# Kernel tuning notes

Hardware: AMD Instinct MI355X
Metric: run time of the kernel (lower is better)

## Reference

```python
import jax, jax.numpy as jnp
import numpy as np
import math

Z, N = 4, 128
EMB, L0, MLPH, GEO = 16, 32, 64, 64
NB, NH = 32, 128
C = MLPH + GEO
BETA, MAXR = 5.0, 10.0
Y0 = 0.5 / math.sqrt(math.pi)  # spherical harmonic l=0


def setup_inputs() -> dict:
    key = jax.random.key(0)
    ks = jax.random.split(key, 24)
    g = lambda i, s: jax.random.normal(ks[i], s, jnp.float32)
    inp = {}
    inp['features'] = jax.random.randint(ks[0], (Z, N, 1), 0, 6)
    inp['geometry'] = g(1, (Z, N, 3))
    inp['mask'] = jnp.ones((Z, N), jnp.float32)
    emb = g(2, (6, EMB))
    inp['emb'] = emb.at[5].set(0.0)  # padding_idx=5
    # radial MLP weights per conv layer (basis->h->h->mul_out*mul_in)
    inp['r0w0'] = g(3, (NB, NH)); inp['r0w1'] = g(4, (NH, NH)); inp['r0w2'] = g(5, (NH, L0 * EMB))
    inp['r1w0'] = g(6, (NB, NH)); inp['r1w1'] = g(7, (NH, NH)); inp['r1w2'] = g(8, (NH, L0 * L0))
    inp['r2w0'] = g(9, (NB, NH)); inp['r2w1'] = g(10, (NH, NH)); inp['r2w2'] = g(11, (NH, MLPH * L0))
    # ResnetPointnet (3 -> GEO per atom, two residual FC blocks)
    inp['pn_w0'] = g(12, (3, GEO)) * 0.3; inp['pn_b0'] = jnp.zeros((GEO,), jnp.float32)
    inp['pn_w1a'] = g(13, (GEO, GEO)) * 0.1; inp['pn_b1a'] = jnp.zeros((GEO,), jnp.float32)
    inp['pn_w1b'] = g(14, (GEO, GEO)) * 0.1; inp['pn_b1b'] = jnp.zeros((GEO,), jnp.float32)
    inp['pn_w2a'] = g(15, (GEO, GEO)) * 0.1; inp['pn_b2a'] = jnp.zeros((GEO,), jnp.float32)
    inp['pn_w2b'] = g(16, (GEO, GEO)) * 0.1; inp['pn_b2b'] = jnp.zeros((GEO,), jnp.float32)
    # output MLP + per-atom BatchNorm1d(natoms) params
    inp['e1_w'] = g(17, (C, C)) * 0.05; inp['e1_b'] = jnp.zeros((C,), jnp.float32)
    inp['bn1_g'] = jnp.ones((N,), jnp.float32); inp['bn1_b'] = jnp.zeros((N,), jnp.float32)
    inp['e2_w'] = g(18, (C, 2 * C)) * 0.05; inp['e2_b'] = jnp.zeros((2 * C,), jnp.float32)
    inp['bn2_g'] = jnp.ones((N,), jnp.float32); inp['bn2_b'] = jnp.zeros((N,), jnp.float32)
    return inp


def _sp(x):
    return jax.nn.softplus(BETA * x) / BETA


def _ssp(x):
    return _sp(x) - math.log(2.0) / BETA


def _leaky(x):
    return jnp.where(x > 0, x, 0.2 * x)


def _radial(radii, w0, w1, w2):
    # CosineBasisModel: smooth cosine^2 bumps then small MLP (e3nn-style /sqrt(fan_in))
    centers = jnp.linspace(0.0, MAXR, NB)
    step = centers[1] - centers[0]
    x = (radii[..., None] - centers) / step
    basis = jnp.where(jnp.abs(x) < 1.0, jnp.cos(0.5 * jnp.pi * x) ** 2, 0.0)  # [z,a,b,NB]
    h = _ssp(basis @ w0 / math.sqrt(NB))
    h = _ssp(h @ w1 / math.sqrt(NH))
    return h @ w2 / math.sqrt(NH)  # [z,a,b,dout*din]


def _bn(x, gamma, beta):
    # torch BatchNorm1d(natoms) on [Z, natoms, C]: normalize over (Z, C) per atom slot
    mu = jnp.mean(x, axis=(0, 2), keepdims=True)
    var = jnp.var(x, axis=(0, 2), keepdims=True)
    xn = (x - mu) * jax.lax.rsqrt(var + 1e-5)
    return xn * gamma[None, :, None] + beta[None, :, None]


def reference(features, geometry, mask, emb,
              r0w0, r0w1, r0w2, r1w0, r1w1, r1w2, r2w0, r2w1, r2w2,
              pn_w0, pn_b0, pn_w1a, pn_b1a, pn_w1b, pn_b1b,
              pn_w2a, pn_b2a, pn_w2b, pn_b2b,
              e1_w, e1_b, bn1_g, bn1_b, e2_w, e2_b, bn2_g, bn2_b):
    # constants(): pairwise geometry, detached in the original
    diff = jax.lax.stop_gradient(geometry[:, None, :, :] - geometry[:, :, None, :])  # [z,a,b,3]
    radii = jnp.linalg.norm(diff, axis=-1)  # [z,a,b]

    # ResnetPointnet: per-atom geometric features
    net = geometry @ pn_w0 + pn_b0
    for (wa, ba, wb, bb) in ((pn_w1a, pn_b1a, pn_w1b, pn_b1b), (pn_w2a, pn_b2a, pn_w2b, pn_b2b)):
        dx = jax.nn.relu(net) @ wa + ba
        dx = jax.nn.relu(dx) @ wb + bb
        net = net + dx
    geo_pn = net * mask[..., None]  # [z,n,GEO]

    # embedding
    f = emb[features[..., 0]]  # [z,n,EMB]

    # equivariant kernel-conv layers; all reps are l=0 so Y = Y0 constant
    dims = ((EMB, L0, r0w0, r0w1, r0w2), (L0, L0, r1w0, r1w1, r1w2), (L0, MLPH, r2w0, r2w1, r2w2))
    for (din, dout, w0, w1, w2) in dims:
        f = f / math.sqrt(N)
        K = _radial(radii, w0, w1, w2).reshape(Z, N, N, dout, din)
        f = jnp.einsum('zabij,zbj,zb->zai', K, f, mask) * Y0
        f = _sp(f)               # GatedBlock with all-scalar Rs -> scalar act only
        f = f * mask[..., None]

    feat = jnp.concatenate([f, geo_pn], axis=2)  # [z,n,C]
    x = _leaky(_bn(feat @ e1_w + e1_b, bn1_g, bn1_b))
    x = _leaky(_bn(x @ e2_w + e2_b, bn2_g, bn2_b))
    out = jnp.sum(x * mask[..., None], axis=1)  # Aggregate(axis=1, sum)
    return out  # [Z, 2*C]
```

## Files before the change

kernel.cpp:

```cpp
#include <hip/hip_runtime.h>
#include <math.h>

#define Zc   4
#define Nc   128
#define EMBc 16
#define L0c  32
#define MLPHc 64
#define GEOc 64
#define NBc  32
#define NHc  128
#define Cc   128
#define SLc  64

typedef float  f32x4  __attribute__((ext_vector_type(4)));
typedef short  bf16x8 __attribute__((ext_vector_type(8)));

union FragU {
    bf16x8 v;
    unsigned short u[8];
    uint2 q2[2];
};

__device__ __forceinline__ float sp5(float x){
    float y = 5.0f * x;
    float t = fabsf(y);
    return (fmaxf(y, 0.0f) + log1pf(__expf(-t))) * 0.2f;
}
__device__ __forceinline__ float ssp5_post(float y){
    float e = __expf(-fabsf(y));
    float u = fmaxf(y, 0.0f) + __logf(1.0f + e);
    return fmaf(0.2f, u, -0.13862943611198906f);
}

__device__ __forceinline__ unsigned int cvtpk_bf16(float a, float b){
    unsigned int r;
    asm("v_cvt_pk_bf16_f32 %0, %1, %2" : "=v"(r) : "v"(a), "v"(b));
    return r;
}
__device__ __forceinline__ unsigned short f2bf(float f){
    unsigned int u = __float_as_uint(f);
    unsigned int r = (u + 0x7FFFu + ((u >> 16) & 1u)) >> 16;
    return (unsigned short)r;
}

__device__ __forceinline__ int kmap(int l, int e){
    return 4*((l >> 4) & 3) + (e & 3) + 16*(e >> 2);
}

__global__ __launch_bounds__(256) void k_init(
    const float* __restrict__ geom, const float* __restrict__ mask,
    const float* __restrict__ pw0, const float* __restrict__ pb0,
    const float* __restrict__ w1a, const float* __restrict__ b1a,
    const float* __restrict__ w1b, const float* __restrict__ b1b,
    const float* __restrict__ w2a, const float* __restrict__ b2a,
    const float* __restrict__ w2b, const float* __restrict__ b2b,
    const int*   __restrict__ features, const float* __restrict__ emb,
    const float* __restrict__ w00, const float* __restrict__ w10,
    const float* __restrict__ w01, const float* __restrict__ w11,
    const float* __restrict__ w02, const float* __restrict__ w12,
    float* __restrict__ geo_pn, float* __restrict__ f0,
    unsigned short* __restrict__ packs, float* __restrict__ outz)
{
    __shared__ float cur[4][GEOc];
    __shared__ float tmp[4][GEOc];
    int bx = blockIdx.x;
    int t  = threadIdx.x;
    if (bx < 128){
        int g  = t >> 6;
        int c  = t & 63;
        int zn = bx*4 + g;
        float gx = geom[zn*3+0], gy = geom[zn*3+1], gz = geom[zn*3+2];
        float v = fmaf(gx, pw0[0*GEOc+c], fmaf(gy, pw0[1*GEOc+c], fmaf(gz, pw0[2*GEOc+c], pb0[c])));
        const float* WA[2] = {w1a, w2a}; const float* BA[2] = {b1a, b2a};
        const float* WB[2] = {w1b, w2b}; const float* BB[2] = {b1b, b2b};
        #pragma unroll
        for (int blk = 0; blk < 2; blk++){
            cur[g][c] = v;
            __syncthreads();
            float s = BA[blk][c];
            for (int k = 0; k < GEOc; k++) s = fmaf(fmaxf(cur[g][k], 0.0f), WA[blk][k*GEOc+c], s);
            tmp[g][c] = s;
            __syncthreads();
            float s2 = BB[blk][c];
            for (int k = 0; k < GEOc; k++) s2 = fmaf(fmaxf(tmp[g][k], 0.0f), WB[blk][k*GEOc+c], s2);
            v = v + s2;
            __syncthreads();
        }
        geo_pn[zn*GEOc + c] = v * mask[zn];
        if (c < EMBc){
            int fi = features[zn];
            f0[zn*EMBc + c] = emb[fi*EMBc + c] * mask[zn] * 0.0022038655607334227f;
        }
    } else if (bx < 368){
        int j = bx - 128;
        int layer = j / 80;
        int sub = j % 80;
        const float* w0s = (layer == 0) ? w00 : (layer == 1) ? w01 : w02;
        const float* w1s = (layer == 0) ? w10 : (layer == 1) ? w11 : w12;
        unsigned short* p0 = packs + layer*4096;
        unsigned short* p1 = packs + 12288 + layer*16384;
        int idx = sub*256 + t;
        if (idx < 4096){
            int t8 = idx >> 9, l = (idx >> 3) & 63, e = idx & 7;
            int k = kmap(l, e);
            int n = (t8 << 4) + (l & 15);
            p0[idx] = f2bf(w0s[k*NHc + n] * 0.8838834764831844f);
        } else {
            int jj = idx - 4096;
            int fid = jj >> 9, l = (jj >> 3) & 63, e = jj & 7;
            int kk = fid >> 3, t8 = fid & 7;
            int k = 32*kk + kmap(l, e);
            int n = 16*t8 + (l & 15);
            p1[jj] = f2bf(w1s[k*NHc + n] * 0.4419417382415922f);
        }
    } else {
        for (int i = t; i < Zc*2*Cc; i += 256) outz[i] = 0.0f;
    }
}

template<int DIN, int DOUT>
__global__ __launch_bounds__(256) void k_gmat(
    const float* __restrict__ f, const float* __restrict__ w2,
    unsigned short* __restrict__ gt)
{
    __shared__ float fsh[8][DIN];
    int t   = threadIdx.x;
    int zb0 = blockIdx.x * 8;
    if (t < 8*DIN){
        int r = t / DIN, j = t % DIN;
        fsh[r][j] = f[(zb0 + r)*DIN + j];
    }
    __syncthreads();
    int mi = blockIdx.y * 256 + t;
    int m_ = mi & (NHc-1);
    int i_ = mi >> 7;
    const float* wrow = w2 + (size_t)(m_*DOUT + i_) * DIN;
    float s[8];
    #pragma unroll
    for (int r = 0; r < 8; r++) s[r] = 0.0f;
    #pragma unroll
    for (int j4 = 0; j4 < DIN/4; j4++){
        float4 w = *reinterpret_cast<const float4*>(&wrow[j4*4]);
        #pragma unroll
        for (int q = 0; q < 4; q++){
            float wv = reinterpret_cast<const float*>(&w)[q];
            int j = j4*4 + q;
            #pragma unroll
            for (int r = 0; r < 8; r++)
                s[r] = fmaf(fsh[r][j], wv, s[r]);
        }
    }
    int z = zb0 >> 7;
    #pragma unroll
    for (int r = 0; r < 8; r++){
        int b = (zb0 + r) & (Nc-1);
        gt[((size_t)z*DOUT + i_)*(Nc*NHc) + b*NHc + m_] = (unsigned short)cvtpk_bf16(s[r], s[r]);
    }
}

template<int DIN, int DOUT>
__global__ __launch_bounds__(256) void k_egmat(
    const float* __restrict__ part, const float* __restrict__ mask,
    const float* __restrict__ w2, unsigned short* __restrict__ gt)
{
    __shared__ float fsh[8][DIN];
    int t   = threadIdx.x;
    int zb0 = blockIdx.x * 8;
    for (int idx = t; idx < 8*DIN; idx += 256){
        int r = idx / DIN, j = idx % DIN;
        int zb = zb0 + r;
        float s = 0.0f;
        #pragma unroll
        for (int sl = 0; sl < SLc; sl++)
            s += part[(size_t)sl*(Zc*Nc*DIN) + zb*DIN + j];
        float m = mask[zb];
        fsh[r][j] = sp5(s) * m * m * 0.0022038655607334227f;
    }
    __syncthreads();
    int mi = blockIdx.y * 256 + t;
    int m_ = mi & (NHc-1);
    int i_ = mi >> 7;
    const float* wrow = w2 + (size_t)(m_*DOUT + i_) * DIN;
    float s[8];
    #pragma unroll
    for (int r = 0; r < 8; r++) s[r] = 0.0f;
    #pragma unroll
    for (int j4 = 0; j4 < DIN/4; j4++){
        float4 w = *reinterpret_cast<const float4*>(&wrow[j4*4]);
        #pragma unroll
        for (int q = 0; q < 4; q++){
            float wv = reinterpret_cast<const float*>(&w)[q];
            int j = j4*4 + q;
            #pragma unroll
            for (int r = 0; r < 8; r++)
                s[r] = fmaf(fsh[r][j], wv, s[r]);
        }
    }
    int z = zb0 >> 7;
    #pragma unroll
    for (int r = 0; r < 8; r++){
        int b = (zb0 + r) & (Nc-1);
        gt[((size_t)z*DOUT + i_)*(Nc*NHc) + b*NHc + m_] = (unsigned short)cvtpk_bf16(s[r], s[r]);
    }
}

__global__ __launch_bounds__(256, 2) void k_pairmlp(
    const float* __restrict__ geom,
    const unsigned short* __restrict__ packs,
    unsigned short* __restrict__ h2all)
{
    __shared__ unsigned short h1s[64*128];
    char* lb = (char*)h1s;
    int t   = threadIdx.x;
    int w   = t >> 6;
    int l   = t & 63;
    int g16 = l >> 4;
    int c   = l & 15;
    int p0  = blockIdx.x * 64;
    int z   = p0 >> 14;
    int a   = (p0 >> 7) & 127;
    int b0  = p0 & 127;

    if (b0 + 16*w + 15 < a) return;

    int layer = blockIdx.y;
    const unsigned short* wp0 = packs + layer*4096;
    const unsigned short* wp1 = packs + 12288 + layer*16384;
    unsigned short* h2 = h2all + (size_t)layer * (Zc*Nc*Nc*NHc);

    int bp = b0 + 16*w + c;
    float ax = geom[(z*Nc + a)*3 + 0];
    float ay = geom[(z*Nc + a)*3 + 1];
    float az = geom[(z*Nc + a)*3 + 2];
    float dx = geom[(z*Nc + bp)*3 + 0] - ax;
    float dy = geom[(z*Nc + bp)*3 + 1] - ay;
    float dz = geom[(z*Nc + bp)*3 + 2] - az;
    float rm = sqrtf(dx*dx + dy*dy + dz*dz);

    FragU af;
    #pragma unroll
    for (int e = 0; e < 8; e++){
        int k = kmap(l, e);
        float x = fmaf(rm, 3.1f, -(float)k);
        float v = 0.0f;
        if (fabsf(x) < 1.0f){ float cc = __cosf(1.57079632679f*x); v = cc*cc; }
        af.u[e] = (unsigned short)cvtpk_bf16(v, v);
    }

    f32x4 acc[8];
    #pragma unroll
    for (int t8 = 0; t8 < 8; t8++) acc[t8] = (f32x4){0.f,0.f,0.f,0.f};
    #pragma unroll
    for (int t8 = 0; t8 < 8; t8++){
        bf16x8 bf = *reinterpret_cast<const bf16x8*>(wp0 + ((t8*64 + l) << 3));
        acc[t8] = __builtin_amdgcn_mfma_f32_16x16x32_bf16(af.v, bf, acc[t8], 0, 0, 0);
    }
    #pragma unroll
    for (int t8 = 0; t8 < 8; t8++){
        #pragma unroll
        for (int rg = 0; rg < 4; rg++){
            int m = 16*w + 4*g16 + rg;
            int n = 16*t8 + c;
            int off = ((m << 8) + (n << 1)) ^ ((m & 7) << 4);
            *(unsigned short*)(lb + off) = (unsigned short)cvtpk_bf16(ssp5_post(acc[t8][rg]), 0.0f);
        }
    }

    f32x4 acc2[8];
    #pragma unroll
    for (int t8 = 0; t8 < 8; t8++) acc2[t8] = (f32x4){0.f,0.f,0.f,0.f};
    int mrow = 16*w + c;
    int sw   = (mrow & 7) << 4;
    #pragma unroll
    for (int kk = 0; kk < 4; kk++){
        int ob = (mrow << 8) + (kk << 6) + (g16 << 3);
        FragU a2;
        a2.q2[0] = *(const uint2*)(lb + (ob ^ sw));
        a2.q2[1] = *(const uint2*)(lb + ((ob + 32) ^ sw));
        #pragma unroll
        for (int t8 = 0; t8 < 8; t8++){
            bf16x8 bf = *reinterpret_cast<const bf16x8*>(wp1 + (((kk*8 + t8)*64 + l) << 3));
            acc2[t8] = __builtin_amdgcn_mfma_f32_16x16x32_bf16(a2.v, bf, acc2[t8], 0, 0, 0);
        }
    }
    size_t zbase = (size_t)z*Nc*Nc*NHc;
    #pragma unroll
    for (int t8 = 0; t8 < 8; t8++){
        #pragma unroll
        for (int rg = 0; rg < 4; rg++){
            int m = 16*w + 4*g16 + rg;
            int b = b0 + m;
            unsigned short val = (unsigned short)cvtpk_bf16(ssp5_post(acc2[t8][rg]), 0.0f);
            h2[zbase + ((size_t)a*Nc + b)*NHc + 16*t8 + c] = val;
            if (b > a)
                h2[zbase + ((size_t)b*Nc + a)*NHc + 16*t8 + c] = val;
        }
    }
}

template<int DOUT>
__global__ __launch_bounds__(256) void k_gemm3m(
    const unsigned short* __restrict__ h2, const unsigned short* __restrict__ gt,
    float* __restrict__ partial)
{
    __shared__ unsigned short Ash[64*256];
    __shared__ unsigned short Bsh[DOUT*256];
    int t = threadIdx.x;
    int w = t >> 6, l = t & 63;
    int g16 = l >> 4, c16 = l & 15;
    int s  = blockIdx.x;
    int at = blockIdx.y;
    int z  = blockIdx.z;
    int a0 = at*64;
    int k0 = s*256;

    {
        const unsigned short* src = h2 + ((size_t)(z*Nc + a0))*(Nc*NHc) + k0;
        #pragma unroll
        for (int it = 0; it < 8; it++){
            int idx = it*256 + t;
            int r = idx >> 5, c8 = idx & 31;
            uint4 v = *reinterpret_cast<const uint4*>(src + (size_t)r*(Nc*NHc) + c8*8);
            int byte = (r*512 + c8*16) ^ ((r & 7) << 4);
            *reinterpret_cast<uint4*>((char*)Ash + byte) = v;
        }
    }
    {
        const unsigned short* src = gt + ((size_t)z*DOUT)*(Nc*NHc) + k0;
        #pragma unroll
        for (int it = 0; it < DOUT/8; it++){
            int idx = it*256 + t;
            int r = idx >> 5, c8 = idx & 31;
            uint4 v = *reinterpret_cast<const uint4*>(src + (size_t)r*(Nc*NHc) + c8*8);
            int byte = (r*512 + c8*16) ^ ((r & 7) << 4);
            *reinterpret_cast<uint4*>((char*)Bsh + byte) = v;
        }
    }
    __syncthreads();

    constexpr int NT = DOUT/16;
    f32x4 acc[NT];
    #pragma unroll
    for (int nt = 0; nt < NT; nt++) acc[nt] = (f32x4){0.f,0.f,0.f,0.f};
    char* Ab = (char*)Ash; char* Bb = (char*)Bsh;
    int ar  = 16*w + c16;
    int asw = (ar & 7) << 4;
    #pragma unroll
    for (int ks = 0; ks < 8; ks++){
        FragU afr;
        int abyte = ar*512 + ks*64 + g16*8;
        afr.q2[0] = *(const uint2*)(Ab + (abyte ^ asw));
        afr.q2[1] = *(const uint2*)(Ab + ((abyte + 32) ^ asw));
        #pragma unroll
        for (int nt = 0; nt < NT; nt++){
            int br  = nt*16 + c16;
            int bsw = (br & 7) << 4;
            int bbyte = br*512 + ks*64 + g16*8;
            FragU bfr;
            bfr.q2[0] = *(const uint2*)(Bb + (bbyte ^ bsw));
            bfr.q2[1] = *(const uint2*)(Bb + ((bbyte + 32) ^ bsw));
            acc[nt] = __builtin_amdgcn_mfma_f32_16x16x32_bf16(afr.v, bfr.v, acc[nt], 0, 0, 0);
        }
    }
    #pragma unroll
    for (int nt = 0; nt < NT; nt++){
        #pragma unroll
        for (int rg = 0; rg < 4; rg++){
            int a = a0 + 16*w + 4*g16 + rg;
            int i = nt*16 + c16;
            partial[(((size_t)s*Zc + z)*Nc + a)*DOUT + i] = acc[nt][rg];
        }
    }
}

__global__ __launch_bounds__(256) void k_tail(
    const float* __restrict__ part, const float* __restrict__ mask,
    const float* __restrict__ geo_pn,
    const float* __restrict__ e1w, const float* __restrict__ e1b,
    const float* __restrict__ g1, const float* __restrict__ b1,
    const float* __restrict__ e2w, const float* __restrict__ e2b,
    const float* __restrict__ g2, const float* __restrict__ b2,
    float* __restrict__ outp)
{
    int n = blockIdx.x;
    int t = threadIdx.x;
    __shared__ float feat[Zc][Cc];
    __shared__ float xln[Zc][Cc];
    __shared__ float r1[4], r2[4];

    {
        int z = t >> 6, i = t & 63;
        float s = 0.0f;
        #pragma unroll
        for (int sl = 0; sl < SLc; sl++)
            s += part[((size_t)sl*Zc*Nc + z*Nc + n)*MLPHc + i];
        float m = mask[z*Nc + n];
        feat[z][i] = sp5(s) * m;
        feat[z][MLPHc + i] = geo_pn[(z*Nc + n)*GEOc + i];
    }
    __syncthreads();

    int c  = t & 127;
    int zh = t >> 7;
    float x1v[2];
    float sum = 0.0f, sq = 0.0f;
    #pragma unroll
    for (int q = 0; q < 2; q++){
        int z = zh*2 + q;
        float s = e1b[c];
        for (int k = 0; k < Cc; k++) s = fmaf(feat[z][k], e1w[k*Cc + c], s);
        x1v[q] = s; sum += s; sq = fmaf(s, s, sq);
    }
    #pragma unroll
    for (int off = 32; off > 0; off >>= 1){
        sum += __shfl_down(sum, off);
        sq  += __shfl_down(sq,  off);
    }
    if ((t & 63) == 0){ r1[t >> 6] = sum; r2[t >> 6] = sq; }
    __syncthreads();
    {
        float tot  = r1[0]+r1[1]+r1[2]+r1[3];
        float totq = r2[0]+r2[1]+r2[2]+r2[3];
        float mu   = tot * (1.0f/512.0f);
        float var  = totq * (1.0f/512.0f) - mu*mu;
        float rstd = rsqrtf(var + 1e-5f);
        float ga = g1[n], be = b1[n];
        #pragma unroll
        for (int q = 0; q < 2; q++){
            float v = (x1v[q] - mu) * rstd * ga + be;
            xln[zh*2 + q][c] = v > 0.0f ? v : 0.2f*v;
        }
    }
    __syncthreads();

    float x2v[4];
    sum = 0.0f; sq = 0.0f;
    #pragma unroll
    for (int z = 0; z < Zc; z++){
        float s = e2b[t];
        for (int k = 0; k < Cc; k++) s = fmaf(xln[z][k], e2w[k*2*Cc + t], s);
        x2v[z] = s; sum += s; sq = fmaf(s, s, sq);
    }
    #pragma unroll
    for (int off = 32; off > 0; off >>= 1){
        sum += __shfl_down(sum, off);
        sq  += __shfl_down(sq,  off);
    }
    if ((t & 63) == 0){ r1[t >> 6] = sum; r2[t >> 6] = sq; }
    __syncthreads();
    {
        float tot  = r1[0]+r1[1]+r1[2]+r1[3];
        float totq = r2[0]+r2[1]+r2[2]+r2[3];
        float mu   = tot * (1.0f/1024.0f);
        float var  = totq * (1.0f/1024.0f) - mu*mu;
        float rstd = rsqrtf(var + 1e-5f);
        float ga = g2[n], be = b2[n];
        #pragma unroll
        for (int z = 0; z < Zc; z++){
            float v = (x2v[z] - mu) * rstd * ga + be;
            v = v > 0.0f ? v : 0.2f*v;
            atomicAdd(&outp[z*2*Cc + t], v * mask[z*Nc + n]);
        }
    }
}

extern "C" void kernel_launch(void* const* d_in, const int* in_sizes, int n_in,
                              void* d_out, int out_size, void* d_ws, size_t ws_size,
                              hipStream_t stream)
{
    const int*   features = (const int*)  d_in[0];
    const float* geom     = (const float*)d_in[1];
    const float* mask     = (const float*)d_in[2];
    const float* emb      = (const float*)d_in[3];
    const float* rw[3][3] = {
        {(const float*)d_in[4],  (const float*)d_in[5],  (const float*)d_in[6]},
        {(const float*)d_in[7],  (const float*)d_in[8],  (const float*)d_in[9]},
        {(const float*)d_in[10], (const float*)d_in[11], (const float*)d_in[12]}};
    const float* pw0 = (const float*)d_in[13]; const float* pb0 = (const float*)d_in[14];
    const float* w1a = (const float*)d_in[15]; const float* b1a = (const float*)d_in[16];
    const float* w1b = (const float*)d_in[17]; const float* b1b = (const float*)d_in[18];
    const float* w2a = (const float*)d_in[19]; const float* b2a = (const float*)d_in[20];
    const float* w2b = (const float*)d_in[21]; const float* b2b = (const float*)d_in[22];
    const float* e1w = (const float*)d_in[23]; const float* e1b = (const float*)d_in[24];
    const float* bn1g= (const float*)d_in[25]; const float* bn1b= (const float*)d_in[26];
    const float* e2w = (const float*)d_in[27]; const float* e2b = (const float*)d_in[28];
    const float* bn2g= (const float*)d_in[29]; const float* bn2b= (const float*)d_in[30];

    float* ws = (float*)d_ws;
    unsigned short* h2buf = (unsigned short*)ws;
    unsigned short* gt    = (unsigned short*)(ws + 12582912);
    float* part   = ws + 12582912 + 2097152;
    float* f0     = part + 2097152;
    float* geo_pn = f0 + 8192;
    unsigned short* packs = (unsigned short*)(geo_pn + 32768);
    (void)ws_size; (void)in_sizes; (void)n_in; (void)out_size;

    const size_t H2L = (size_t)Zc*Nc*Nc*NHc;

    k_init<<<369, 256, 0, stream>>>(geom, mask, pw0, pb0, w1a, b1a, w1b, b1b,
                                    w2a, b2a, w2b, b2b, features, emb,
                                    rw[0][0], rw[0][1], rw[1][0], rw[1][1],
                                    rw[2][0], rw[2][1],
                                    geo_pn, f0, packs, (float*)d_out);
    k_pairmlp<<<dim3(Zc*Nc*Nc/64, 3), 256, 0, stream>>>(geom, packs, h2buf);

    k_gmat<16,32><<<dim3(Zc*Nc/8, (NHc*32)/256), 256, 0, stream>>>(f0, rw[0][2], gt);
    k_gemm3m<32><<<dim3(SLc,2,Zc), 256, 0, stream>>>(h2buf, gt, part);
    k_egmat<32,32><<<dim3(Zc*Nc/8, (NHc*32)/256), 256, 0, stream>>>(part, mask, rw[1][2], gt);
    k_gemm3m<32><<<dim3(SLc,2,Zc), 256, 0, stream>>>(h2buf + H2L, gt, part);
    k_egmat<32,64><<<dim3(Zc*Nc/8, (NHc*64)/256), 256, 0, stream>>>(part, mask, rw[2][2], gt);
    k_gemm3m<64><<<dim3(SLc,2,Zc), 256, 0, stream>>>(h2buf + 2*H2L, gt, part);

    k_tail<<<Nc, 256, 0, stream>>>(part, mask, geo_pn, e1w, e1b, bn1g, bn1b,
                                   e2w, e2b, bn2g, bn2b, (float*)d_out);
}
```

Before: 152.3 us.

## Fuse all stages into one cooperative persistent kernel with grid syncs

Replaces the nine separate kernel launches with a single cooperative kernel of 512 blocks. The blocks loop over virtual block indices for each stage and separate the stages with grid.sync(), which removes the per-launch gaps and tail effects between small stages. The K-split of the h2·G GEMM is also halved from 256 to 128 columns, which gives 128 partial slices. That means more, smaller GEMM blocks, a doubled partial buffer and twice as many partials to reduce in the egmat and tail stages. If cooperative launch is unavailable, the code falls back to the multi-kernel path.

```diff
diff --git a/kernel.cpp b/kernel.cpp
--- a/kernel.cpp
+++ b/kernel.cpp
@@ -1,5 +1,8 @@
 #include <hip/hip_runtime.h>
+#include <hip/hip_cooperative_groups.h>
 #include <math.h>
+
+namespace cg = cooperative_groups;
 
 #define Zc   4
 #define Nc   128
@@ -10,7 +13,8 @@
 #define NBc  32
 #define NHc  128
 #define Cc   128
-#define SLc  64
+#define SLc  128
+#define SL2  128
 
 typedef float  f32x4  __attribute__((ext_vector_type(4)));
 typedef short  bf16x8 __attribute__((ext_vector_type(8)));
@@ -21,6 +25,16 @@
     uint2 q2[2];
 };
 
+struct P {
+    const float *geom, *mask, *emb;
+    const int*   features;
+    const float *pw0,*pb0,*w1a,*b1a,*w1b,*b1b,*w2a,*b2a,*w2b,*b2b;
+    const float *r00,*r01,*r02, *r10,*r11,*r12, *r20,*r21,*r22;
+    const float *e1w,*e1b,*bn1g,*bn1b,*e2w,*e2b,*bn2g,*bn2b;
+    unsigned short *h2buf, *gt, *packs;
+    float *part, *f0, *geo_pn, *outp;
+};
+
 __device__ __forceinline__ float sp5(float x){
     float y = 5.0f * x;
     float t = fabsf(y);
@@ -31,7 +45,6 @@
     float u = fmaxf(y, 0.0f) + __logf(1.0f + e);
     return fmaf(0.2f, u, -0.13862943611198906f);
 }
-
 __device__ __forceinline__ unsigned int cvtpk_bf16(float a, float b){
     unsigned int r;
     asm("v_cvt_pk_bf16_f32 %0, %1, %2" : "=v"(r) : "v"(a), "v"(b));
@@ -42,63 +55,52 @@
     unsigned int r = (u + 0x7FFFu + ((u >> 16) & 1u)) >> 16;
     return (unsigned short)r;
 }
-
 __device__ __forceinline__ int kmap(int l, int e){
     return 4*((l >> 4) & 3) + (e & 3) + 16*(e >> 2);
 }
 
-__global__ __launch_bounds__(256) void k_init(
-    const float* __restrict__ geom, const float* __restrict__ mask,
-    const float* __restrict__ pw0, const float* __restrict__ pb0,
-    const float* __restrict__ w1a, const float* __restrict__ b1a,
-    const float* __restrict__ w1b, const float* __restrict__ b1b,
-    const float* __restrict__ w2a, const float* __restrict__ b2a,
-    const float* __restrict__ w2b, const float* __restrict__ b2b,
-    const int*   __restrict__ features, const float* __restrict__ emb,
-    const float* __restrict__ w00, const float* __restrict__ w10,
-    const float* __restrict__ w01, const float* __restrict__ w11,
-    const float* __restrict__ w02, const float* __restrict__ w12,
-    float* __restrict__ geo_pn, float* __restrict__ f0,
-    unsigned short* __restrict__ packs, float* __restrict__ outz)
-{
-    __shared__ float cur[4][GEOc];
-    __shared__ float tmp[4][GEOc];
-    int bx = blockIdx.x;
-    int t  = threadIdx.x;
+__device__ void init_dev(int bx, const P& p, char* smem)
+{
+    float* cur = (float*)smem;
+    float* tmp = cur + 4*GEOc;
+    int t = threadIdx.x;
     if (bx < 128){
         int g  = t >> 6;
         int c  = t & 63;
         int zn = bx*4 + g;
-        float gx = geom[zn*3+0], gy = geom[zn*3+1], gz = geom[zn*3+2];
-        float v = fmaf(gx, pw0[0*GEOc+c], fmaf(gy, pw0[1*GEOc+c], fmaf(gz, pw0[2*GEOc+c], pb0[c])));
-        const float* WA[2] = {w1a, w2a}; const float* BA[2] = {b1a, b2a};
-        const float* WB[2] = {w1b, w2b}; const float* BB[2] = {b1b, b2b};
+        float gx = p.geom[zn*3+0], gy = p.geom[zn*3+1], gz = p.geom[zn*3+2];
+        float v = fmaf(gx, p.pw0[0*GEOc+c], fmaf(gy, p.pw0[1*GEOc+c],
+                  fmaf(gz, p.pw0[2*GEOc+c], p.pb0[c])));
+        const float* WA[2] = {p.w1a, p.w2a}; const float* BA[2] = {p.b1a, p.b2a};
+        const float* WB[2] = {p.w1b, p.w2b}; const float* BB[2] = {p.b1b, p.b2b};
         #pragma unroll
         for (int blk = 0; blk < 2; blk++){
-            cur[g][c] = v;
+            cur[g*GEOc + c] = v;
             __syncthreads();
             float s = BA[blk][c];
-            for (int k = 0; k < GEOc; k++) s = fmaf(fmaxf(cur[g][k], 0.0f), WA[blk][k*GEOc+c], s);
-            tmp[g][c] = s;
+            for (int k = 0; k < GEOc; k++)
+                s = fmaf(fmaxf(cur[g*GEOc + k], 0.0f), WA[blk][k*GEOc+c], s);
+            tmp[g*GEOc + c] = s;
             __syncthreads();
             float s2 = BB[blk][c];
-            for (int k = 0; k < GEOc; k++) s2 = fmaf(fmaxf(tmp[g][k], 0.0f), WB[blk][k*GEOc+c], s2);
+            for (int k = 0; k < GEOc; k++)
+                s2 = fmaf(fmaxf(tmp[g*GEOc + k], 0.0f), WB[blk][k*GEOc+c], s2);
             v = v + s2;
             __syncthreads();
         }
-        geo_pn[zn*GEOc + c] = v * mask[zn];
+        p.geo_pn[zn*GEOc + c] = v * p.mask[zn];
         if (c < EMBc){
-            int fi = features[zn];
-            f0[zn*EMBc + c] = emb[fi*EMBc + c] * mask[zn] * 0.0022038655607334227f;
+            int fi = p.features[zn];
+            p.f0[zn*EMBc + c] = p.emb[fi*EMBc + c] * p.mask[zn] * 0.0022038655607334227f;
         }
     } else if (bx < 368){
         int j = bx - 128;
         int layer = j / 80;
         int sub = j % 80;
-        const float* w0s = (layer == 0) ? w00 : (layer == 1) ? w01 : w02;
-        const float* w1s = (layer == 0) ? w10 : (layer == 1) ? w11 : w12;
-        unsigned short* p0 = packs + layer*4096;
-        unsigned short* p1 = packs + 12288 + layer*16384;
+        const float* w0s = (layer == 0) ? p.r00 : (layer == 1) ? p.r10 : p.r20;
+        const float* w1s = (layer == 0) ? p.r01 : (layer == 1) ? p.r11 : p.r21;
+        unsigned short* p0 = p.packs + layer*4096;
+        unsigned short* p1 = p.packs + 12288 + layer*16384;
         int idx = sub*256 + t;
         if (idx < 4096){
             int t8 = idx >> 9, l = (idx >> 3) & 63, e = idx & 7;
@@ -114,127 +116,37 @@
             p1[jj] = f2bf(w1s[k*NHc + n] * 0.4419417382415922f);
         }
     } else {
-        for (int i = t; i < Zc*2*Cc; i += 256) outz[i] = 0.0f;
-    }
-}
-
-template<int DIN, int DOUT>
-__global__ __launch_bounds__(256) void k_gmat(
-    const float* __restrict__ f, const float* __restrict__ w2,
-    unsigned short* __restrict__ gt)
-{
-    __shared__ float fsh[8][DIN];
-    int t   = threadIdx.x;
-    int zb0 = blockIdx.x * 8;
-    if (t < 8*DIN){
-        int r = t / DIN, j = t % DIN;
-        fsh[r][j] = f[(zb0 + r)*DIN + j];
-    }
-    __syncthreads();
-    int mi = blockIdx.y * 256 + t;
-    int m_ = mi & (NHc-1);
-    int i_ = mi >> 7;
-    const float* wrow = w2 + (size_t)(m_*DOUT + i_) * DIN;
-    float s[8];
-    #pragma unroll
-    for (int r = 0; r < 8; r++) s[r] = 0.0f;
-    #pragma unroll
-    for (int j4 = 0; j4 < DIN/4; j4++){
-        float4 w = *reinterpret_cast<const float4*>(&wrow[j4*4]);
-        #pragma unroll
-        for (int q = 0; q < 4; q++){
-            float wv = reinterpret_cast<const float*>(&w)[q];
-            int j = j4*4 + q;
-            #pragma unroll
-            for (int r = 0; r < 8; r++)
-                s[r] = fmaf(fsh[r][j], wv, s[r]);
-        }
-    }
-    int z = zb0 >> 7;
-    #pragma unroll
-    for (int r = 0; r < 8; r++){
-        int b = (zb0 + r) & (Nc-1);
-        gt[((size_t)z*DOUT + i_)*(Nc*NHc) + b*NHc + m_] = (unsigned short)cvtpk_bf16(s[r], s[r]);
-    }
-}
-
-template<int DIN, int DOUT>
-__global__ __launch_bounds__(256) void k_egmat(
-    const float* __restrict__ part, const float* __restrict__ mask,
-    const float* __restrict__ w2, unsigned short* __restrict__ gt)
-{
-    __shared__ float fsh[8][DIN];
-    int t   = threadIdx.x;
-    int zb0 = blockIdx.x * 8;
-    for (int idx = t; idx < 8*DIN; idx += 256){
-        int r = idx / DIN, j = idx % DIN;
-        int zb = zb0 + r;
-        float s = 0.0f;
-        #pragma unroll
-        for (int sl = 0; sl < SLc; sl++)
-            s += part[(size_t)sl*(Zc*Nc*DIN) + zb*DIN + j];
-        float m = mask[zb];
-        fsh[r][j] = sp5(s) * m * m * 0.0022038655607334227f;
-    }
-    __syncthreads();
-    int mi = blockIdx.y * 256 + t;
-    int m_ = mi & (NHc-1);
-    int i_ = mi >> 7;
-    const float* wrow = w2 + (size_t)(m_*DOUT + i_) * DIN;
-    float s[8];
-    #pragma unroll
-    for (int r = 0; r < 8; r++) s[r] = 0.0f;
-    #pragma unroll
-    for (int j4 = 0; j4 < DIN/4; j4++){
-        float4 w = *reinterpret_cast<const float4*>(&wrow[j4*4]);
-        #pragma unroll
-        for (int q = 0; q < 4; q++){
-            float wv = reinterpret_cast<const float*>(&w)[q];
-            int j = j4*4 + q;
-            #pragma unroll
-            for (int r = 0; r < 8; r++)
-                s[r] = fmaf(fsh[r][j], wv, s[r]);
-        }
-    }
-    int z = zb0 >> 7;
-    #pragma unroll
-    for (int r = 0; r < 8; r++){
-        int b = (zb0 + r) & (Nc-1);
-        gt[((size_t)z*DOUT + i_)*(Nc*NHc) + b*NHc + m_] = (unsigned short)cvtpk_bf16(s[r], s[r]);
-    }
-}
-
-__global__ __launch_bounds__(256, 2) void k_pairmlp(
-    const float* __restrict__ geom,
-    const unsigned short* __restrict__ packs,
-    unsigned short* __restrict__ h2all)
-{
-    __shared__ unsigned short h1s[64*128];
-    char* lb = (char*)h1s;
+        for (int i = t; i < Zc*2*Cc; i += 256) p.outp[i] = 0.0f;
+    }
+}
+
+__device__ void pairmlp_dev(int vb, const P& p, char* smem)
+{
+    char* lb = smem;
     int t   = threadIdx.x;
     int w   = t >> 6;
     int l   = t & 63;
     int g16 = l >> 4;
     int c   = l & 15;
-    int p0  = blockIdx.x * 64;
+    int layer = vb >> 10;
+    int p0  = (vb & 1023) * 64;
     int z   = p0 >> 14;
     int a   = (p0 >> 7) & 127;
     int b0  = p0 & 127;
 
     if (b0 + 16*w + 15 < a) return;
 
-    int layer = blockIdx.y;
-    const unsigned short* wp0 = packs + layer*4096;
-    const unsigned short* wp1 = packs + 12288 + layer*16384;
-    unsigned short* h2 = h2all + (size_t)layer * (Zc*Nc*Nc*NHc);
+    const unsigned short* wp0 = p.packs + layer*4096;
+    const unsigned short* wp1 = p.packs + 12288 + layer*16384;
+    unsigned short* h2 = p.h2buf + (size_t)layer * ((size_t)Zc*Nc*Nc*NHc);
 
     int bp = b0 + 16*w + c;
-    float ax = geom[(z*Nc + a)*3 + 0];
-    float ay = geom[(z*Nc + a)*3 + 1];
-    float az = geom[(z*Nc + a)*3 + 2];
-    float dx = geom[(z*Nc + bp)*3 + 0] - ax;
-    float dy = geom[(z*Nc + bp)*3 + 1] - ay;
-    float dz = geom[(z*Nc + bp)*3 + 2] - az;
+    float ax = p.geom[(z*Nc + a)*3 + 0];
+    float ay = p.geom[(z*Nc + a)*3 + 1];
+    float az = p.geom[(z*Nc + a)*3 + 2];
+    float dx = p.geom[(z*Nc + bp)*3 + 0] - ax;
+    float dy = p.geom[(z*Nc + bp)*3 + 1] - ay;
+    float dz = p.geom[(z*Nc + bp)*3 + 2] - az;
     float rm = sqrtf(dx*dx + dy*dy + dz*dz);
 
     FragU af;
@@ -298,41 +210,131 @@
     }
 }
 
-template<int DOUT>
-__global__ __launch_bounds__(256) void k_gemm3m(
-    const unsigned short* __restrict__ h2, const unsigned short* __restrict__ gt,
-    float* __restrict__ partial)
-{
-    __shared__ unsigned short Ash[64*256];
-    __shared__ unsigned short Bsh[DOUT*256];
+template<int DIN, int DOUT>
+__device__ void gmat_dev(int vb, const float* f, const float* w2,
+                         unsigned short* gt, char* smem)
+{
+    float (*fsh)[DIN] = (float (*)[DIN])smem;
+    int t  = threadIdx.x;
+    int bx = vb & 63, by = vb >> 6;
+    int zb0 = bx * 8;
+    if (t < 8*DIN){
+        int r = t / DIN, j = t % DIN;
+        fsh[r][j] = f[(zb0 + r)*DIN + j];
+    }
+    __syncthreads();
+    int mi = by * 256 + t;
+    int m_ = mi & (NHc-1);
+    int i_ = mi >> 7;
+    const float* wrow = w2 + (size_t)(m_*DOUT + i_) * DIN;
+    float s[8];
+    #pragma unroll
+    for (int r = 0; r < 8; r++) s[r] = 0.0f;
+    #pragma unroll
+    for (int j4 = 0; j4 < DIN/4; j4++){
+        float4 wv4 = *reinterpret_cast<const float4*>(&wrow[j4*4]);
+        #pragma unroll
+        for (int q = 0; q < 4; q++){
+            float wv = reinterpret_cast<const float*>(&wv4)[q];
+            int j = j4*4 + q;
+            #pragma unroll
+            for (int r = 0; r < 8; r++)
+                s[r] = fmaf(fsh[r][j], wv, s[r]);
+        }
+    }
+    int z = zb0 >> 7;
+    #pragma unroll
+    for (int r = 0; r < 8; r++){
+        int b = (zb0 + r) & (Nc-1);
+        gt[((size_t)z*DOUT + i_)*(Nc*NHc) + b*NHc + m_] = (unsigned short)cvtpk_bf16(s[r], s[r]);
+    }
+    __syncthreads();
+}
+
+template<int DIN, int DOUT>
+__device__ void egmat_dev(int vb, const float* part, const float* mask,
+                          const float* w2, unsigned short* gt, char* smem)
+{
+    float (*fsh)[DIN] = (float (*)[DIN])smem;
+    int t  = threadIdx.x;
+    int bx = vb & 63, by = vb >> 6;
+    int zb0 = bx * 8;
+    for (int idx = t; idx < 8*DIN; idx += 256){
+        int r = idx / DIN, j = idx % DIN;
+        int zb = zb0 + r;
+        float s = 0.0f;
+        for (int sl = 0; sl < SLc; sl++)
+            s += part[(size_t)sl*(Zc*Nc*DIN) + zb*DIN + j];
+        float m = mask[zb];
+        fsh[r][j] = sp5(s) * m * m * 0.0022038655607334227f;
+    }
+    __syncthreads();
+    int mi = by * 256 + t;
+    int m_ = mi & (NHc-1);
+    int i_ = mi >> 7;
+    const float* wrow = w2 + (size_t)(m_*DOUT + i_) * DIN;
+    float s[8];
+    #pragma unroll
+    for (int r = 0; r < 8; r++) s[r] = 0.0f;
+    #pragma unroll
+    for (int j4 = 0; j4 < DIN/4; j4++){
+        float4 wv4 = *reinterpret_cast<const float4*>(&wrow[j4*4]);
+        #pragma unroll
+        for (int q = 0; q < 4; q++){
+            float wv = reinterpret_cast<const float*>(&wv4)[q];
+            int j = j4*4 + q;
+            #pragma unroll
+            for (int r = 0; r < 8; r++)
+                s[r] = fmaf(fsh[r][j], wv, s[r]);
+        }
+    }
+    int z = zb0 >> 7;
+    #pragma unroll
+    for (int r = 0; r < 8; r++){
+        int b = (zb0 + r) & (Nc-1);
+        gt[((size_t)z*DOUT + i_)*(Nc*NHc) + b*NHc + m_] = (unsigned short)cvtpk_bf16(s[r], s[r]);
+    }
+    __syncthreads();
+}
+
+template<int DOUT, int KS>
+__device__ void gemm3_dev(int vb, const unsigned short* h2, const unsigned short* gt,
+                          float* partial, char* smem)
+{
+    constexpr int NS   = (Nc*NHc)/KS;
+    constexpr int ROWB = KS*2;
+    unsigned short* Ash = (unsigned short*)smem;
+    unsigned short* Bsh = (unsigned short*)(smem + 64*ROWB);
     int t = threadIdx.x;
     int w = t >> 6, l = t & 63;
     int g16 = l >> 4, c16 = l & 15;
-    int s  = blockIdx.x;
-    int at = blockIdx.y;
-    int z  = blockIdx.z;
+    int s  = vb % NS;
+    int at = (vb / NS) & 1;
+    int z  = vb / (NS*2);
     int a0 = at*64;
-    int k0 = s*256;
+    int k0 = s*KS;
 
     {
         const unsigned short* src = h2 + ((size_t)(z*Nc + a0))*(Nc*NHc) + k0;
-        #pragma unroll
-        for (int it = 0; it < 8; it++){
+        constexpr int ITA = (64*(KS/8))/256;
+        #pragma unroll
+        for (int it = 0; it < ITA; it++){
             int idx = it*256 + t;
-            int r = idx >> 5, c8 = idx & 31;
+            int r = idx / (KS/8), c8 = idx % (KS/8);
             uint4 v = *reinterpret_cast<const uint4*>(src + (size_t)r*(Nc*NHc) + c8*8);
-            int byte = (r*512 + c8*16) ^ ((r & 7) << 4);
+            int byte = (r*ROWB + c8*16) ^ ((r & 7) << 4);
             *reinterpret_cast<uint4*>((char*)Ash + byte) = v;
         }
     }
     {
         const unsigned short* src = gt + ((size_t)z*DOUT)*(Nc*NHc) + k0;
-        #pragma unroll
-        for (int it = 0; it < DOUT/8; it++){
+        constexpr int ITB = (DOUT*(KS/8))/256;
+        #pragma unroll
+        for (int it = 0; it < ITB; it++){
             int idx = it*256 + t;
-            int r = idx >> 5, c8 = idx & 31;
+            int r = idx / (KS/8), c8 = idx % (KS/8);
             uint4 v = *reinterpret_cast<const uint4*>(src + (size_t)r*(Nc*NHc) + c8*8);
-            int byte = (r*512 + c8*16) ^ ((r & 7) << 4);
+            int byte = (r*ROWB + c8*16) ^ ((r & 7) << 4);
             *reinterpret_cast<uint4*>((char*)Bsh + byte) = v;
         }
     }
@@ -342,23 +344,22 @@
     f32x4 acc[NT];
     #pragma unroll
     for (int nt = 0; nt < NT; nt++) acc[nt] = (f32x4){0.f,0.f,0.f,0.f};
-    char* Ab = (char*)Ash; char* Bb = (char*)Bsh;
     int ar  = 16*w + c16;
     int asw = (ar & 7) << 4;
     #pragma unroll
-    for (int ks = 0; ks < 8; ks++){
+    for (int ks = 0; ks < KS/32; ks++){
         FragU afr;
-        int abyte = ar*512 + ks*64 + g16*8;
-        afr.q2[0] = *(const uint2*)(Ab + (abyte ^ asw));
-        afr.q2[1] = *(const uint2*)(Ab + ((abyte + 32) ^ asw));
+        int abyte = ar*ROWB + ks*64 + g16*8;
+        afr.q2[0] = *(const uint2*)((char*)Ash + (abyte ^ asw));
+        afr.q2[1] = *(const uint2*)((char*)Ash + ((abyte + 32) ^ asw));
         #pragma unroll
         for (int nt = 0; nt < NT; nt++){
             int br  = nt*16 + c16;
             int bsw = (br & 7) << 4;
-            int bbyte = br*512 + ks*64 + g16*8;
+            int bbyte = br*ROWB + ks*64 + g16*8;
             FragU bfr;
-            bfr.q2[0] = *(const uint2*)(Bb + (bbyte ^ bsw));
-            bfr.q2[1] = *(const uint2*)(Bb + ((bbyte + 32) ^ bsw));
+            bfr.q2[0] = *(const uint2*)((char*)Bsh + (bbyte ^ bsw));
+            bfr.q2[1] = *(const uint2*)((char*)Bsh + ((bbyte + 32) ^ bsw));
             acc[nt] = __builtin_amdgcn_mfma_f32_16x16x32_bf16(afr.v, bfr.v, acc[nt], 0, 0, 0);
         }
     }
@@ -371,32 +372,25 @@
             partial[(((size_t)s*Zc + z)*Nc + a)*DOUT + i] = acc[nt][rg];
         }
     }
-}
-
-__global__ __launch_bounds__(256) void k_tail(
-    const float* __restrict__ part, const float* __restrict__ mask,
-    const float* __restrict__ geo_pn,
-    const float* __restrict__ e1w, const float* __restrict__ e1b,
-    const float* __restrict__ g1, const float* __restrict__ b1,
-    const float* __restrict__ e2w, const float* __restrict__ e2b,
-    const float* __restrict__ g2, const float* __restrict__ b2,
-    float* __restrict__ outp)
-{
-    int n = blockIdx.x;
+    __syncthreads();
+}
+
+__device__ void tail_dev(int n, const P& p, char* smem)
+{
+    float* feat = (float*)smem;
+    float* xln  = feat + Zc*Cc;
+    float* r1   = xln + Zc*Cc;
+    float* r2   = r1 + 4;
     int t = threadIdx.x;
-    __shared__ float feat[Zc][Cc];
-    __shared__ float xln[Zc][Cc];
-    __shared__ float r1[4], r2[4];
 
     {
         int z = t >> 6, i = t & 63;
         float s = 0.0f;
-        #pragma unroll
-        for (int sl = 0; sl < SLc; sl++)
-            s += part[((size_t)sl*Zc*Nc + z*Nc + n)*MLPHc + i];
-        float m = mask[z*Nc + n];
-        feat[z][i] = sp5(s) * m;
-        feat[z][MLPHc + i] = geo_pn[(z*Nc + n)*GEOc + i];
+        for (int sl = 0; sl < SL2; sl++)
+            s += p.part[((size_t)sl*Zc*Nc + z*Nc + n)*MLPHc + i];
+        float m = p.mask[z*Nc + n];
+        feat[z*Cc + i] = sp5(s) * m;
+        feat[z*Cc + MLPHc + i] = p.geo_pn[(z*Nc + n)*GEOc + i];
     }
     __syncthreads();
 
@@ -407,8 +401,8 @@
     #pragma unroll
     for (int q = 0; q < 2; q++){
         int z = zh*2 + q;
-        float s = e1b[c];
-        for (int k = 0; k < Cc; k++) s = fmaf(feat[z][k], e1w[k*Cc + c], s);
+        float s = p.e1b[c];
+        for (int k = 0; k < Cc; k++) s = fmaf(feat[z*Cc + k], p.e1w[k*Cc + c], s);
         x1v[q] = s; sum += s; sq = fmaf(s, s, sq);
     }
     #pragma unroll
@@ -424,11 +418,11 @@
         float mu   = tot * (1.0f/512.0f);
         float var  = totq * (1.0f/512.0f) - mu*mu;
         float rstd = rsqrtf(var + 1e-5f);
-        float ga = g1[n], be = b1[n];
+        float ga = p.bn1g[n], be = p.bn1b[n];
         #pragma unroll
         for (int q = 0; q < 2; q++){
             float v = (x1v[q] - mu) * rstd * ga + be;
-            xln[zh*2 + q][c] = v > 0.0f ? v : 0.2f*v;
+            xln[(zh*2 + q)*Cc + c] = v > 0.0f ? v : 0.2f*v;
         }
     }
     __syncthreads();
@@ -437,8 +431,8 @@
     sum = 0.0f; sq = 0.0f;
     #pragma unroll
     for (int z = 0; z < Zc; z++){
-        float s = e2b[t];
-        for (int k = 0; k < Cc; k++) s = fmaf(xln[z][k], e2w[k*2*Cc + t], s);
+        float s = p.e2b[t];
+        for (int k = 0; k < Cc; k++) s = fmaf(xln[z*Cc + k], p.e2w[k*2*Cc + t], s);
         x2v[z] = s; sum += s; sq = fmaf(s, s, sq);
     }
     #pragma unroll
@@ -454,63 +448,129 @@
         float mu   = tot * (1.0f/1024.0f);
         float var  = totq * (1.0f/1024.0f) - mu*mu;
         float rstd = rsqrtf(var + 1e-5f);
-        float ga = g2[n], be = b2[n];
+        float ga = p.bn2g[n], be = p.bn2b[n];
         #pragma unroll
         for (int z = 0; z < Zc; z++){
             float v = (x2v[z] - mu) * rstd * ga + be;
             v = v > 0.0f ? v : 0.2f*v;
-            atomicAdd(&outp[z*2*Cc + t], v * mask[z*Nc + n]);
-        }
-    }
+            atomicAdd(&p.outp[z*2*Cc + t], v * p.mask[z*Nc + n]);
+        }
+    }
+}
+
+__global__ __launch_bounds__(256, 2) void k_mono(P p)
+{
+    __shared__ __align__(16) char smem[32768];
+    cg::grid_group grid = cg::this_grid();
+    const size_t H2L = (size_t)Zc*Nc*Nc*NHc;
+    int bid = blockIdx.x;
+
+    if (bid < 369) init_dev(bid, p, smem);
+    grid.sync();
+
+    for (int vb = bid; vb < 3072; vb += 512) pairmlp_dev(vb, p, smem);
+    grid.sync();
+
+    for (int vb = bid; vb < 1024; vb += 512) gmat_dev<16,32>(vb, p.f0, p.r02, p.gt, smem);
+    grid.sync();
+    for (int vb = bid; vb < 1024; vb += 512) gemm3_dev<32,128>(vb, p.h2buf, p.gt, p.part, smem);
+    grid.sync();
+    for (int vb = bid; vb < 1024; vb += 512) egmat_dev<32,32>(vb, p.part, p.mask, p.r12, p.gt, smem);
+    grid.sync();
+    for (int vb = bid; vb < 1024; vb += 512) gemm3_dev<32,128>(vb, p.h2buf + H2L, p.gt, p.part, smem);
+    grid.sync();
+    for (int vb = bid; vb < 2048; vb += 512) egmat_dev<32,64>(vb, p.part, p.mask, p.r22, p.gt, smem);
+    grid.sync();
+    for (int vb = bid; vb < 1024; vb += 512) gemm3_dev<64,128>(vb, p.h2buf + 2*H2L, p.gt, p.part, smem);
+    grid.sync();
+
+    if (bid < 128) tail_dev(bid, p, smem);
+}
+
+__global__ __launch_bounds__(256) void k_init_g(P p){
+    __shared__ __align__(16) char smem[2048];
+    init_dev(blockIdx.x, p, smem);
+}
+__global__ __launch_bounds__(256, 2) void k_pairmlp_g(P p){
+    __shared__ __align__(16) char smem[16384];
+    pairmlp_dev(blockIdx.y*1024 + blockIdx.x, p, smem);
+}
+template<int DIN, int DOUT>
+__global__ __launch_bounds__(256) void k_gmat_g(P p, const float* f, const float* w2){
+    __shared__ __align__(16) char smem[8*DIN*4];
+    gmat_dev<DIN,DOUT>(blockIdx.y*64 + blockIdx.x, f, w2, p.gt, smem);
+}
+template<int DIN, int DOUT>
+__global__ __launch_bounds__(256) void k_egmat_g(P p, const float* w2){
+    __shared__ __align__(16) char smem[8*DIN*4];
+    egmat_dev<DIN,DOUT>(blockIdx.y*64 + blockIdx.x, p.part, p.mask, w2, p.gt, smem);
+}
+template<int DOUT, int KS>
+__global__ __launch_bounds__(256) void k_gemm3_g(P p, const unsigned short* h2){
+    __shared__ __align__(16) char smem[(64+DOUT)*KS*2];
+    constexpr int NS = (Nc*NHc)/KS;
+    int vb = (blockIdx.z*2 + blockIdx.y)*NS + blockIdx.x;
+    gemm3_dev<DOUT,KS>(vb, h2, p.gt, p.part, smem);
+}
+__global__ __launch_bounds__(256) void k_tail_g(P p){
+    __shared__ __align__(16) char smem[4224];
+    tail_dev(blockIdx.x, p, smem);
 }
 
 extern "C" void kernel_launch(void* const* d_in, const int* in_sizes, int n_in,
                               void* d_out, int out_size, void* d_ws, size_t ws_size,
                               hipStream_t stream)
 {
-    const int*   features = (const int*)  d_in[0];
-    const float* geom     = (const float*)d_in[1];
-    const float* mask     = (const float*)d_in[2];
-    const float* emb      = (const float*)d_in[3];
-    const float* rw[3][3] = {
-        {(const float*)d_in[4],  (const float*)d_in[5],  (const float*)d_in[6]},
-        {(const float*)d_in[7],  (const float*)d_in[8],  (const float*)d_in[9]},
-        {(const float*)d_in[10], (const float*)d_in[11], (const float*)d_in[12]}};
-    const float* pw0 = (const float*)d_in[13]; const float* pb0 = (const float*)d_in[14];
-    const float* w1a = (const float*)d_in[15]; const float* b1a = (const float*)d_in[16];
-    const float* w1b = (const float*)d_in[17]; const float* b1b = (const float*)d_in[18];
-    const float* w2a = (const float*)d_in[19]; const float* b2a = (const float*)d_in[20];
-    const float* w2b = (const float*)d_in[21]; const float* b2b = (const float*)d_in[22];
-    const float* e1w = (const float*)d_in[23]; const float* e1b = (const float*)d_in[24];
-    const float* bn1g= (const float*)d_in[25]; const float* bn1b= (const float*)d_in[26];
-    const float* e2w = (const float*)d_in[27]; const float* e2b = (const float*)d_in[28];
-    const float* bn2g= (const float*)d_in[29]; const float* bn2b= (const float*)d_in[30];
+    P p;
+    p.features = (const int*)  d_in[0];
+    p.geom     = (const float*)d_in[1];
+    p.mask     = (const float*)d_in[2];
+    p.emb      = (const float*)d_in[3];
+    p.r00 = (const float*)d_in[4];  p.r01 = (const float*)d_in[5];  p.r02 = (const float*)d_in[6];
+    p.r10 = (const float*)d_in[7];  p.r11 = (const float*)d_in[8];  p.r12 = (const float*)d_in[9];
+    p.r20 = (const float*)d_in[10]; p.r21 = (const float*)d_in[11]; p.r22 = (const float*)d_in[12];
+    p.pw0 = (const float*)d_in[13]; p.pb0 = (const float*)d_in[14];
+    p.w1a = (const float*)d_in[15]; p.b1a = (const float*)d_in[16];
+    p.w1b = (const float*)d_in[17]; p.b1b = (const float*)d_in[18];
+    p.w2a = (const float*)d_in[19]; p.b2a = (const float*)d_in[20];
+    p.w2b = (const float*)d_in[21]; p.b2b = (const float*)d_in[22];
+    p.e1w = (const float*)d_in[23]; p.e1b = (const float*)d_in[24];
+    p.bn1g= (const float*)d_in[25]; p.bn1b= (const float*)d_in[26];
+    p.e2w = (const float*)d_in[27]; p.e2b = (const float*)d_in[28];
+    p.bn2g= (const float*)d_in[29]; p.bn2b= (const float*)d_in[30];
 
     float* ws = (float*)d_ws;
-    unsigned short* h2buf = (unsigned short*)ws;
-    unsigned short* gt    = (unsigned short*)(ws + 12582912);
-    float* part   = ws + 12582912 + 2097152;
-    float* f0     = part + 2097152;
-    float* geo_pn = f0 + 8192;
-    unsigned short* packs = (unsigned short*)(geo_pn + 32768);
+    p.h2buf = (unsigned short*)ws;
+    p.gt    = (unsigned short*)(ws + 12582912);
+    p.part  = ws + 12582912 + 2097152;
+    p.f0    = p.part + 4194304;
+    p.geo_pn= p.f0 + 8192;
+    p.packs = (unsigned short*)(p.geo_pn + 32768);
+    p.outp  = (float*)d_out;
     (void)ws_size; (void)in_sizes; (void)n_in; (void)out_size;
 
+    int dev = 0; hipGetDevice(&dev);
+    int coop = 0; hipDeviceGetAttribute(&coop, hipDeviceAttributeCooperativeLaunch, dev);
+    int maxBlocks = 0;
+    hipOccupancyMaxActiveBlocksPerMultiprocessor(&maxBlocks, k_mono, 256, 0);
+
+    bool launched = false;
+    if (coop != 0 && maxBlocks >= 2){
+        void* args[] = { (void*)&p };
+        hipError_t e = hipLaunchCooperativeKernel((void*)k_mono, dim3(512), dim3(256),
+                                                  args, 0, stream);
+        launched = (e == hipSuccess);
+    }
+    if (launched) return;
+
     const size_t H2L = (size_t)Zc*Nc*Nc*NHc;
-
-    k_init<<<369, 256, 0, stream>>>(geom, mask, pw0, pb0, w1a, b1a, w1b, b1b,
-                                    w2a, b2a, w2b, b2b, features, emb,
-                                    rw[0][0], rw[0][1], rw[1][0], rw[1][1],
-                                    rw[2][0], rw[2][1],
-                                    geo_pn, f0, packs, (float*)d_out);
-    k_pairmlp<<<dim3(Zc*Nc*Nc/64, 3), 256, 0, stream>>>(geom, packs, h2buf);
-
-    k_gmat<16,32><<<dim3(Zc*Nc/8, (NHc*32)/256), 256, 0, stream>>>(f0, rw[0][2], gt);
-    k_gemm3m<32><<<dim3(SLc,2,Zc), 256, 0, stream>>>(h2buf, gt, part);
-    k_egmat<32,32><<<dim3(Zc*Nc/8, (NHc*32)/256), 256, 0, stream>>>(part, mask, rw[1][2], gt);
-    k_gemm3m<32><<<dim3(SLc,2,Zc), 256, 0, stream>>>(h2buf + H2L, gt, part);
-    k_egmat<32,64><<<dim3(Zc*Nc/8, (NHc*64)/256), 256, 0, stream>>>(part, mask, rw[2][2], gt);
-    k_gemm3m<64><<<dim3(SLc,2,Zc), 256, 0, stream>>>(h2buf + 2*H2L, gt, part);
-
-    k_tail<<<Nc, 256, 0, stream>>>(part, mask, geo_pn, e1w, e1b, bn1g, bn1b,
-                                   e2w, e2b, bn2g, bn2b, (float*)d_out);
-}
+    k_init_g<<<369, 256, 0, stream>>>(p);
+    k_pairmlp_g<<<dim3(1024, 3), 256, 0, stream>>>(p);
+    k_gmat_g<16,32><<<dim3(64, 16), 256, 0, stream>>>(p, p.f0, p.r02);
+    k_gemm3_g<32,128><<<dim3(128, 2, Zc), 256, 0, stream>>>(p, p.h2buf);
+    k_egmat_g<32,32><<<dim3(64, 16), 256, 0, stream>>>(p, p.r12);
+    k_gemm3_g<32,128><<<dim3(128, 2, Zc), 256, 0, stream>>>(p, p.h2buf + H2L);
+    k_egmat_g<32,64><<<dim3(64, 32), 256, 0, stream>>>(p, p.r22);
+    k_gemm3_g<64,128><<<dim3(128, 2, Zc), 256, 0, stream>>>(p, p.h2buf + 2*H2L);
+    k_tail_g<<<128, 256, 0, stream>>>(p);
+}
```

Measured after the change: 200.4 us. 31.6% more time.
